# Kernel optimization log

Measured on AMD Instinct MI355X. Metric: run time of the kernel, lower is better.

The kernel has to match this reference:

```python
import jax, jax.numpy as jnp
import numpy as np

SCALING = 32.0 / 16.0  # alpha / rank

def setup_inputs() -> dict:
    key = jax.random.key(0)
    k1, k2, k3, k4 = jax.random.split(key, 4)
    B_, S, D_in, D_out, R = 4, 4096, 2048, 2048, 16
    x = jax.random.normal(k1, (B_, S, D_in), dtype=jnp.float32)
    # dequantized 4-bit base weight, torch Linear layout [out, in]
    W_base = jax.random.normal(k2, (D_out, D_in), dtype=jnp.float32) * 0.02
    A = jax.random.normal(k3, (R, D_in), dtype=jnp.float32) * (1.0 / np.sqrt(D_in))
    # torch code zero-inits lora_B, but use random for nontrivial gradient checking
    B = jax.random.normal(k4, (D_out, R), dtype=jnp.float32) * 0.02
    return {"x": x, "W_base": W_base, "A": A, "B": B}

def reference(x, W_base, A, B):
    # base: Y = x @ W_base^T   [b, s, out]
    base = jnp.einsum('bsd,od->bso', x, W_base)
    # LoRA: (x @ A^T) @ B^T * scaling   (rank is tiny, keep factored)
    lora = jnp.einsum('bsr,or->bso', jnp.einsum('bsd,rd->bsr', x, A), B)
    return base + lora * SCALING
```

## Files before the change

kernel.cpp:

```cpp
#include <hip/hip_runtime.h>


typedef __bf16 bf16x8 __attribute__((ext_vector_type(8)));
typedef float  f32x4  __attribute__((ext_vector_type(4)));
typedef unsigned short u16x8 __attribute__((ext_vector_type(8)));

#define AS1C(p) ((const __attribute__((address_space(1))) void*)(p))
#define AS3(p)  ((__attribute__((address_space(3))) void*)(p))

__device__ __forceinline__ unsigned short f2bf(float f) {
  unsigned int u = __float_as_uint(f);
  u += 0x7FFFu + ((u >> 16) & 1u);
  return (unsigned short)(u >> 16);
}

constexpr int M_ = 16384;
constexpr int N_ = 2048;
constexpr int K_ = 2048;
constexpr int R_ = 16;
constexpr float SCALING = 2.0f;

constexpr int BM = 128, BN = 128, BK = 32;

__global__ __launch_bounds__(256) void cvt_kernel(const float* __restrict__ in,
                                                  unsigned short* __restrict__ out) {
  size_t i = (size_t)blockIdx.x * blockDim.x + threadIdx.x;
  const float4* p = (const float4*)in;
  float4 a = p[2 * i];
  float4 b = p[2 * i + 1];
  u16x8 o;
  o[0] = f2bf(a.x); o[1] = f2bf(a.y); o[2] = f2bf(a.z); o[3] = f2bf(a.w);
  o[4] = f2bf(b.x); o[5] = f2bf(b.y); o[6] = f2bf(b.z); o[7] = f2bf(b.w);
  ((u16x8*)out)[i] = o;
}

__global__ __launch_bounds__(256) void weff_kernel(const float* __restrict__ W,
                                                   const float* __restrict__ A,
                                                   const float* __restrict__ Bl,
                                                   unsigned short* __restrict__ out) {
  int idx = blockIdx.x * blockDim.x + threadIdx.x;
  int o = idx >> 11;
  int d = idx & 2047;
  float acc = W[idx];
#pragma unroll
  for (int r = 0; r < R_; ++r)
    acc = fmaf(SCALING * Bl[o * R_ + r], A[r * K_ + d], acc);
  out[idx] = f2bf(acc);
}

__global__ __launch_bounds__(256) void gemm_kernel(const unsigned short* __restrict__ X,
                                                   const unsigned short* __restrict__ W,
                                                   float* __restrict__ C) {
  __shared__ __align__(16) unsigned short As[BM * BK];
  __shared__ __align__(16) unsigned short Bs[BN * BK];

  const int tid  = threadIdx.x;
  const int wave = tid >> 6;
  const int lane = tid & 63;

  const int bm = blockIdx.y * BM;
  const int bn = blockIdx.x * BN;

  const int wm = (wave & 1) * 64;
  const int wn = (wave >> 1) * 64;

  f32x4 acc[4][4] = {};

  const int rq = lane >> 2;
  const int sg = lane & 3;

  const unsigned short* xg0 = X + (size_t)(bm + wave * 32 + rq) * K_ + sg * 8;
  const unsigned short* xg1 = X + (size_t)(bm + wave * 32 + 16 + rq) * K_ + sg * 8;
  const unsigned short* wg0 = W + (size_t)(bn + wave * 32 + rq) * K_ + sg * 8;
  const unsigned short* wg1 = W + (size_t)(bn + wave * 32 + 16 + rq) * K_ + sg * 8;

  unsigned short* la0 = &As[(wave * 32) * BK];
  unsigned short* la1 = &As[(wave * 32 + 16) * BK];
  unsigned short* lb0 = &Bs[(wave * 32) * BK];
  unsigned short* lb1 = &Bs[(wave * 32 + 16) * BK];

  const int fm = lane & 15;
  const int fk = (lane >> 4) * 8;

  for (int k0 = 0; k0 < K_; k0 += BK) {
    __builtin_amdgcn_global_load_lds(AS1C(xg0 + k0), AS3(la0), 16, 0, 0);
    __builtin_amdgcn_global_load_lds(AS1C(xg1 + k0), AS3(la1), 16, 0, 0);
    __builtin_amdgcn_global_load_lds(AS1C(wg0 + k0), AS3(lb0), 16, 0, 0);
    __builtin_amdgcn_global_load_lds(AS1C(wg1 + k0), AS3(lb1), 16, 0, 0);
    __syncthreads();

    bf16x8 af[4], bf[4];
#pragma unroll
    for (int i = 0; i < 4; ++i)
      af[i] = *(const bf16x8*)&As[(wm + i * 16 + fm) * BK + fk];
#pragma unroll
    for (int j = 0; j < 4; ++j)
      bf[j] = *(const bf16x8*)&Bs[(wn + j * 16 + fm) * BK + fk];

#pragma unroll
    for (int i = 0; i < 4; ++i)
#pragma unroll
      for (int j = 0; j < 4; ++j)
        acc[i][j] = __builtin_amdgcn_mfma_f32_16x16x32_bf16(af[i], bf[j], acc[i][j], 0, 0, 0);

    __syncthreads();
  }

  const int r0   = (lane >> 4) * 4;
  const int col0 = lane & 15;
#pragma unroll
  for (int i = 0; i < 4; ++i) {
#pragma unroll
    for (int j = 0; j < 4; ++j) {
      size_t base = (size_t)(bm + wm + i * 16 + r0) * N_ + (size_t)(bn + wn + j * 16 + col0);
#pragma unroll
      for (int r = 0; r < 4; ++r)
        C[base + (size_t)r * N_] = acc[i][j][r];
    }
  }
}

extern "C" void kernel_launch(void* const* d_in, const int* in_sizes, int n_in,
                              void* d_out, int out_size, void* d_ws, size_t ws_size,
                              hipStream_t stream) {
  const float* x  = (const float*)d_in[0];
  const float* W  = (const float*)d_in[1];
  const float* A  = (const float*)d_in[2];
  const float* Bl = (const float*)d_in[3];
  float* out = (float*)d_out;

  unsigned short* Xb   = (unsigned short*)d_ws;
  unsigned short* Weff = Xb + (size_t)M_ * K_;

  cvt_kernel<<<(M_ * (size_t)K_) / 8 / 256, 256, 0, stream>>>(x, Xb);

  weff_kernel<<<(N_ * K_) / 256, 256, 0, stream>>>(W, A, Bl, Weff);

  dim3 grid(N_ / BN, M_ / BM);
  gemm_kernel<<<grid, 256, 0, stream>>>(Xb, Weff, out);
}
```

Measured before the change: 445.4 us.

## Fuse fp32-to-bf16 conversion of x into GEMM A-tile loads, remap tiles per XCD

Removes the separate conversion kernel, so the GEMM now reads fp32 x directly, rounds it to bf16 in registers (round-half-up) and writes it into a padded LDS tile. This avoids writing and re-reading a 64MB bf16 copy of x. It also remaps block IDs so that each XCD works on a contiguous band of M rows, aiming for better L2 reuse. In exchange, every N-tile block now reads x at fp32 width, which is 16x redundant traffic that depends on the cache, and the direct-to-LDS load for A is lost, leaving the K loop synchronous.

```diff
diff --git a/kernel.cpp b/kernel.cpp
--- a/kernel.cpp
+++ b/kernel.cpp
@@ -8,10 +8,13 @@
 #define AS1C(p) ((const __attribute__((address_space(1))) void*)(p))
 #define AS3(p)  ((__attribute__((address_space(3))) void*)(p))
 
-__device__ __forceinline__ unsigned short f2bf(float f) {
+__device__ __forceinline__ unsigned short f2bf_rne(float f) {
   unsigned int u = __float_as_uint(f);
   u += 0x7FFFu + ((u >> 16) & 1u);
   return (unsigned short)(u >> 16);
+}
+__device__ __forceinline__ unsigned short f2bf_rhu(float f) {
+  return (unsigned short)((__float_as_uint(f) + 0x8000u) >> 16);
 }
 
 constexpr int M_ = 16384;
@@ -21,18 +24,7 @@
 constexpr float SCALING = 2.0f;
 
 constexpr int BM = 128, BN = 128, BK = 32;
-
-__global__ __launch_bounds__(256) void cvt_kernel(const float* __restrict__ in,
-                                                  unsigned short* __restrict__ out) {
-  size_t i = (size_t)blockIdx.x * blockDim.x + threadIdx.x;
-  const float4* p = (const float4*)in;
-  float4 a = p[2 * i];
-  float4 b = p[2 * i + 1];
-  u16x8 o;
-  o[0] = f2bf(a.x); o[1] = f2bf(a.y); o[2] = f2bf(a.z); o[3] = f2bf(a.w);
-  o[4] = f2bf(b.x); o[5] = f2bf(b.y); o[6] = f2bf(b.z); o[7] = f2bf(b.w);
-  ((u16x8*)out)[i] = o;
-}
+constexpr int APAD = 40;
 
 __global__ __launch_bounds__(256) void weff_kernel(const float* __restrict__ W,
                                                    const float* __restrict__ A,
@@ -45,37 +37,41 @@
 #pragma unroll
   for (int r = 0; r < R_; ++r)
     acc = fmaf(SCALING * Bl[o * R_ + r], A[r * K_ + d], acc);
-  out[idx] = f2bf(acc);
+  out[idx] = f2bf_rne(acc);
 }
 
-__global__ __launch_bounds__(256) void gemm_kernel(const unsigned short* __restrict__ X,
+__global__ __launch_bounds__(256) void gemm_kernel(const float* __restrict__ X,
                                                    const unsigned short* __restrict__ W,
                                                    float* __restrict__ C) {
-  __shared__ __align__(16) unsigned short As[BM * BK];
+  __shared__ __align__(16) unsigned short As[BM * APAD];
   __shared__ __align__(16) unsigned short Bs[BN * BK];
 
   const int tid  = threadIdx.x;
   const int wave = tid >> 6;
   const int lane = tid & 63;
 
-  const int bm = blockIdx.y * BM;
-  const int bn = blockIdx.x * BN;
+  const int id   = blockIdx.x + gridDim.x * blockIdx.y;
+  const int xcd  = id & 7;
+  const int slot = id >> 3;
+  const int bm   = (xcd * 16 + (slot >> 4)) * BM;
+  const int bn   = (slot & 15) * BN;
 
   const int wm = (wave & 1) * 64;
   const int wn = (wave >> 1) * 64;
 
   f32x4 acc[4][4] = {};
 
+  const int rr  = tid >> 2;
+  const int sg2 = tid & 3;
+  const float* xg0 = X + (size_t)(bm + rr) * K_ + sg2 * 8;
+  const float* xg1 = X + (size_t)(bm + 64 + rr) * K_ + sg2 * 8;
+  unsigned short* wA0 = &As[rr * APAD + sg2 * 8];
+  unsigned short* wA1 = &As[(rr + 64) * APAD + sg2 * 8];
+
   const int rq = lane >> 2;
   const int sg = lane & 3;
-
-  const unsigned short* xg0 = X + (size_t)(bm + wave * 32 + rq) * K_ + sg * 8;
-  const unsigned short* xg1 = X + (size_t)(bm + wave * 32 + 16 + rq) * K_ + sg * 8;
   const unsigned short* wg0 = W + (size_t)(bn + wave * 32 + rq) * K_ + sg * 8;
   const unsigned short* wg1 = W + (size_t)(bn + wave * 32 + 16 + rq) * K_ + sg * 8;
-
-  unsigned short* la0 = &As[(wave * 32) * BK];
-  unsigned short* la1 = &As[(wave * 32 + 16) * BK];
   unsigned short* lb0 = &Bs[(wave * 32) * BK];
   unsigned short* lb1 = &Bs[(wave * 32 + 16) * BK];
 
@@ -83,25 +79,36 @@
   const int fk = (lane >> 4) * 8;
 
   for (int k0 = 0; k0 < K_; k0 += BK) {
-    __builtin_amdgcn_global_load_lds(AS1C(xg0 + k0), AS3(la0), 16, 0, 0);
-    __builtin_amdgcn_global_load_lds(AS1C(xg1 + k0), AS3(la1), 16, 0, 0);
+    float4 a0 = *(const float4*)(xg0 + k0);
+    float4 a1 = *(const float4*)(xg0 + k0 + 4);
+    float4 b0 = *(const float4*)(xg1 + k0);
+    float4 b1 = *(const float4*)(xg1 + k0 + 4);
     __builtin_amdgcn_global_load_lds(AS1C(wg0 + k0), AS3(lb0), 16, 0, 0);
     __builtin_amdgcn_global_load_lds(AS1C(wg1 + k0), AS3(lb1), 16, 0, 0);
+
+    u16x8 pa, pb;
+    pa[0] = f2bf_rhu(a0.x); pa[1] = f2bf_rhu(a0.y); pa[2] = f2bf_rhu(a0.z); pa[3] = f2bf_rhu(a0.w);
+    pa[4] = f2bf_rhu(a1.x); pa[5] = f2bf_rhu(a1.y); pa[6] = f2bf_rhu(a1.z); pa[7] = f2bf_rhu(a1.w);
+    pb[0] = f2bf_rhu(b0.x); pb[1] = f2bf_rhu(b0.y); pb[2] = f2bf_rhu(b0.z); pb[3] = f2bf_rhu(b0.w);
+    pb[4] = f2bf_rhu(b1.x); pb[5] = f2bf_rhu(b1.y); pb[6] = f2bf_rhu(b1.z); pb[7] = f2bf_rhu(b1.w);
+    *(u16x8*)wA0 = pa;
+    *(u16x8*)wA1 = pb;
+
     __syncthreads();
 
-    bf16x8 af[4], bf[4];
+    bf16x8 af[4], bfr[4];
 #pragma unroll
     for (int i = 0; i < 4; ++i)
-      af[i] = *(const bf16x8*)&As[(wm + i * 16 + fm) * BK + fk];
+      af[i] = *(const bf16x8*)&As[(wm + i * 16 + fm) * APAD + fk];
 #pragma unroll
     for (int j = 0; j < 4; ++j)
-      bf[j] = *(const bf16x8*)&Bs[(wn + j * 16 + fm) * BK + fk];
+      bfr[j] = *(const bf16x8*)&Bs[(wn + j * 16 + fm) * BK + fk];
 
 #pragma unroll
     for (int i = 0; i < 4; ++i)
 #pragma unroll
       for (int j = 0; j < 4; ++j)
-        acc[i][j] = __builtin_amdgcn_mfma_f32_16x16x32_bf16(af[i], bf[j], acc[i][j], 0, 0, 0);
+        acc[i][j] = __builtin_amdgcn_mfma_f32_16x16x32_bf16(af[i], bfr[j], acc[i][j], 0, 0, 0);
 
     __syncthreads();
   }
@@ -129,13 +136,10 @@
   const float* Bl = (const float*)d_in[3];
   float* out = (float*)d_out;
 
-  unsigned short* Xb   = (unsigned short*)d_ws;
-  unsigned short* Weff = Xb + (size_t)M_ * K_;
-
-  cvt_kernel<<<(M_ * (size_t)K_) / 8 / 256, 256, 0, stream>>>(x, Xb);
+  unsigned short* Weff = (unsigned short*)d_ws;
 
   weff_kernel<<<(N_ * K_) / 256, 256, 0, stream>>>(W, A, Bl, Weff);
 
   dim3 grid(N_ / BN, M_ / BM);
-  gemm_kernel<<<grid, 256, 0, stream>>>(Xb, Weff, out);
+  gemm_kernel<<<grid, 256, 0, stream>>>(x, Weff, out);
 }
```

New measurement: 452.5 us. No clear change (+1.6%).

## Double K tile, swizzle LDS layout, remap blocks per XCD, nontemporal stores

Applied to the files above, without the earlier changes.

Raises BK from 32 to 64, which halves the number of barrier-separated K iterations in the GEMM. A rotated (XOR-like) segment swizzle is applied to both the global-to-LDS loads and the fragment reads to avoid LDS bank conflicts. Block IDs are remapped so that each XCD works on a contiguous band of M rows, improving L2 reuse of X tiles. Output stores become nontemporal. The cost is double the LDS per block, which may lower occupancy, and the remap assumes a round-robin dispatch across 8 XCDs.

```diff
diff --git a/kernel.cpp b/kernel.cpp
--- a/kernel.cpp
+++ b/kernel.cpp
@@ -8,7 +8,7 @@
 #define AS1C(p) ((const __attribute__((address_space(1))) void*)(p))
 #define AS3(p)  ((__attribute__((address_space(3))) void*)(p))
 
-__device__ __forceinline__ unsigned short f2bf(float f) {
+__device__ __forceinline__ unsigned short f2bf_rne(float f) {
   unsigned int u = __float_as_uint(f);
   u += 0x7FFFu + ((u >> 16) & 1u);
   return (unsigned short)(u >> 16);
@@ -20,7 +20,7 @@
 constexpr int R_ = 16;
 constexpr float SCALING = 2.0f;
 
-constexpr int BM = 128, BN = 128, BK = 32;
+constexpr int BM = 128, BN = 128, BK = 64;
 
 __global__ __launch_bounds__(256) void cvt_kernel(const float* __restrict__ in,
                                                   unsigned short* __restrict__ out) {
@@ -29,8 +29,8 @@
   float4 a = p[2 * i];
   float4 b = p[2 * i + 1];
   u16x8 o;
-  o[0] = f2bf(a.x); o[1] = f2bf(a.y); o[2] = f2bf(a.z); o[3] = f2bf(a.w);
-  o[4] = f2bf(b.x); o[5] = f2bf(b.y); o[6] = f2bf(b.z); o[7] = f2bf(b.w);
+  o[0] = f2bf_rne(a.x); o[1] = f2bf_rne(a.y); o[2] = f2bf_rne(a.z); o[3] = f2bf_rne(a.w);
+  o[4] = f2bf_rne(b.x); o[5] = f2bf_rne(b.y); o[6] = f2bf_rne(b.z); o[7] = f2bf_rne(b.w);
   ((u16x8*)out)[i] = o;
 }
 
@@ -45,7 +45,7 @@
 #pragma unroll
   for (int r = 0; r < R_; ++r)
     acc = fmaf(SCALING * Bl[o * R_ + r], A[r * K_ + d], acc);
-  out[idx] = f2bf(acc);
+  out[idx] = f2bf_rne(acc);
 }
 
 __global__ __launch_bounds__(256) void gemm_kernel(const unsigned short* __restrict__ X,
@@ -58,56 +58,62 @@
   const int wave = tid >> 6;
   const int lane = tid & 63;
 
-  const int bm = blockIdx.y * BM;
-  const int bn = blockIdx.x * BN;
+  const int id   = blockIdx.x + gridDim.x * blockIdx.y;
+  const int xcd  = id & 7;
+  const int slot = id >> 3;
+  const int bm   = (xcd * 16 + (slot >> 4)) * BM;
+  const int bn   = (slot & 15) * BN;
 
   const int wm = (wave & 1) * 64;
   const int wn = (wave >> 1) * 64;
 
   f32x4 acc[4][4] = {};
 
-  const int rq = lane >> 2;
-  const int sg = lane & 3;
+  const int r8 = lane >> 3;
+  const int gseg = ((lane & 7) - r8) & 7;
 
-  const unsigned short* xg0 = X + (size_t)(bm + wave * 32 + rq) * K_ + sg * 8;
-  const unsigned short* xg1 = X + (size_t)(bm + wave * 32 + 16 + rq) * K_ + sg * 8;
-  const unsigned short* wg0 = W + (size_t)(bn + wave * 32 + rq) * K_ + sg * 8;
-  const unsigned short* wg1 = W + (size_t)(bn + wave * 32 + 16 + rq) * K_ + sg * 8;
+  const unsigned short* xst = X + (size_t)(bm + wave * 32 + r8) * K_ + gseg * 8;
+  const unsigned short* wst = W + (size_t)(bn + wave * 32 + r8) * K_ + gseg * 8;
+  unsigned short* lA = &As[(wave * 32) * BK];
+  unsigned short* lB = &Bs[(wave * 32) * BK];
 
-  unsigned short* la0 = &As[(wave * 32) * BK];
-  unsigned short* la1 = &As[(wave * 32 + 16) * BK];
-  unsigned short* lb0 = &Bs[(wave * 32) * BK];
-  unsigned short* lb1 = &Bs[(wave * 32 + 16) * BK];
-
-  const int fm = lane & 15;
-  const int fk = (lane >> 4) * 8;
+  const int fm   = lane & 15;
+  const int quad = lane >> 4;
 
   for (int k0 = 0; k0 < K_; k0 += BK) {
-    __builtin_amdgcn_global_load_lds(AS1C(xg0 + k0), AS3(la0), 16, 0, 0);
-    __builtin_amdgcn_global_load_lds(AS1C(xg1 + k0), AS3(la1), 16, 0, 0);
-    __builtin_amdgcn_global_load_lds(AS1C(wg0 + k0), AS3(lb0), 16, 0, 0);
-    __builtin_amdgcn_global_load_lds(AS1C(wg1 + k0), AS3(lb1), 16, 0, 0);
+#pragma unroll
+    for (int c = 0; c < 4; ++c)
+      __builtin_amdgcn_global_load_lds(AS1C(xst + (size_t)(c * 8) * K_ + k0),
+                                       AS3(lA + c * 8 * BK), 16, 0, 0);
+#pragma unroll
+    for (int c = 0; c < 4; ++c)
+      __builtin_amdgcn_global_load_lds(AS1C(wst + (size_t)(c * 8) * K_ + k0),
+                                       AS3(lB + c * 8 * BK), 16, 0, 0);
     __syncthreads();
 
-    bf16x8 af[4], bf[4];
 #pragma unroll
-    for (int i = 0; i < 4; ++i)
-      af[i] = *(const bf16x8*)&As[(wm + i * 16 + fm) * BK + fk];
+    for (int t = 0; t < 2; ++t) {
+      const int sp = ((4 * t + quad + fm) & 7) * 8;
+      bf16x8 af[4], bfr[4];
 #pragma unroll
-    for (int j = 0; j < 4; ++j)
-      bf[j] = *(const bf16x8*)&Bs[(wn + j * 16 + fm) * BK + fk];
+      for (int i = 0; i < 4; ++i)
+        af[i] = *(const bf16x8*)&As[(wm + i * 16 + fm) * BK + sp];
+#pragma unroll
+      for (int j = 0; j < 4; ++j)
+        bfr[j] = *(const bf16x8*)&Bs[(wn + j * 16 + fm) * BK + sp];
 
 #pragma unroll
-    for (int i = 0; i < 4; ++i)
+      for (int i = 0; i < 4; ++i)
 #pragma unroll
-      for (int j = 0; j < 4; ++j)
-        acc[i][j] = __builtin_amdgcn_mfma_f32_16x16x32_bf16(af[i], bf[j], acc[i][j], 0, 0, 0);
+        for (int j = 0; j < 4; ++j)
+          acc[i][j] = __builtin_amdgcn_mfma_f32_16x16x32_bf16(af[i], bfr[j], acc[i][j], 0, 0, 0);
+    }
 
     __syncthreads();
   }
 
-  const int r0   = (lane >> 4) * 4;
-  const int col0 = lane & 15;
+  const int r0   = quad * 4;
+  const int col0 = fm;
 #pragma unroll
   for (int i = 0; i < 4; ++i) {
 #pragma unroll
@@ -115,7 +121,7 @@
       size_t base = (size_t)(bm + wm + i * 16 + r0) * N_ + (size_t)(bn + wn + j * 16 + col0);
 #pragma unroll
       for (int r = 0; r < 4; ++r)
-        C[base + (size_t)r * N_] = acc[i][j][r];
+        __builtin_nontemporal_store(acc[i][j][r], &C[base + (size_t)r * N_]);
     }
   }
 }
@@ -132,8 +138,7 @@
   unsigned short* Xb   = (unsigned short*)d_ws;
   unsigned short* Weff = Xb + (size_t)M_ * K_;
 
-  cvt_kernel<<<(M_ * (size_t)K_) / 8 / 256, 256, 0, stream>>>(x, Xb);
-
+  cvt_kernel<<<(int)((size_t)M_ * K_ / 8 / 256), 256, 0, stream>>>(x, Xb);
   weff_kernel<<<(N_ * K_) / 256, 256, 0, stream>>>(W, A, Bl, Weff);
 
   dim3 grid(N_ / BN, M_ / BM);
```

Result: faster. 379.8 us (-14.7%).
